# Kernel tuning notes

Hardware: AMD Instinct MI355X
Metric: run time of the kernel (lower is better)

The kernel has to match this reference:

```python
import jax, jax.numpy as jnp
import numpy as np

B, N = 8, 261888
PRE_NMS_LIMIT = 6000
PROPOSAL_COUNT = 1000
SCORE_THRES = 0.5
NMS_IOU_THRES = 0.7
RPN_BBOX_STD_DEV = jnp.asarray([0.1, 0.1, 0.2, 0.2], dtype=jnp.float32)
EPS = 1e-8


def setup_inputs() -> dict:
    key = jax.random.key(0)
    k1, k2, k3, k4 = jax.random.split(key, 4)
    # class scores: softmax over (negative, positive) logits
    logits = jax.random.normal(k1, (B, N, 2), dtype=jnp.float32)
    rpn_probs = jax.nn.softmax(logits, axis=-1)
    # raw (normalized) bbox deltas; layer multiplies by RPN_BBOX_STD_DEV
    rpn_bbox = jax.random.normal(k2, (B, N, 4), dtype=jnp.float32)
    # valid normalized anchors: y1<y2, x1<x2, roughly inside [0,1]
    ctr = jax.random.uniform(k3, (B, N, 2), minval=0.05, maxval=0.95, dtype=jnp.float32)
    size = jax.random.uniform(k4, (B, N, 2), minval=0.02, maxval=0.25, dtype=jnp.float32)
    anchors = jnp.concatenate([ctr - 0.5 * size, ctr + 0.5 * size], axis=-1)  # (y1,x1,y2,x2)
    return {"rpn_probs": rpn_probs, "rpn_bbox": rpn_bbox, "anchors": anchors}


def _apply_box_deltas(boxes, deltas):
    # boxes: [..., (y1,x1,y2,x2)], deltas: [..., (dy,dx,log(dh),log(dw))]
    h = boxes[..., 2] - boxes[..., 0]
    w = boxes[..., 3] - boxes[..., 1]
    cy = boxes[..., 0] + 0.5 * h
    cx = boxes[..., 1] + 0.5 * w
    cy = cy + deltas[..., 0] * h
    cx = cx + deltas[..., 1] * w
    h = h * jnp.exp(deltas[..., 2])
    w = w * jnp.exp(deltas[..., 3])
    y1 = cy - 0.5 * h
    x1 = cx - 0.5 * w
    return jnp.stack([y1, x1, y1 + h, x1 + w], axis=-1)


def _iou_one_vs_all(box, boxes, areas):
    # box: [4], boxes: [M,4], areas: [M]
    yy1 = jnp.maximum(box[0], boxes[:, 0])
    xx1 = jnp.maximum(box[1], boxes[:, 1])
    yy2 = jnp.minimum(box[2], boxes[:, 2])
    xx2 = jnp.minimum(box[3], boxes[:, 3])
    inter = jnp.maximum(yy2 - yy1, 0.0) * jnp.maximum(xx2 - xx1, 0.0)
    area_b = (box[2] - box[0]) * (box[3] - box[1])
    return inter / (area_b + areas - inter + EPS)


def _nms_single(boxes, scores):
    # boxes: [M,4] clipped to [0,1]; scores: [M]
    areas = (boxes[:, 2] - boxes[:, 0]) * (boxes[:, 3] - boxes[:, 1])
    live = jnp.where(scores >= SCORE_THRES, scores, -1.0)

    def step(s, _):
        idx = jnp.argmax(s)
        ok = s[idx] > 0.0
        box = boxes[idx]
        iou = _iou_one_vs_all(box, boxes, areas)
        s_new = jnp.where(iou >= NMS_IOU_THRES, -1.0, s)  # self has iou=1 -> suppressed
        s_new = s_new.at[idx].set(-1.0)
        out_box = jnp.where(ok, box, jnp.zeros((4,), boxes.dtype))
        return s_new, out_box

    _, picked = jax.lax.scan(step, live, None, length=PROPOSAL_COUNT)
    return picked  # [PROPOSAL_COUNT, 4], zero-padded


def reference(rpn_probs, rpn_bbox, anchors):
    scores = rpn_probs[..., 1]                                   # [B,N]
    deltas = rpn_bbox * RPN_BBOX_STD_DEV.reshape(1, 1, 4)        # [B,N,4]
    pre_nms = min(PRE_NMS_LIMIT, scores.shape[1])
    top_scores, ix = jax.lax.top_k(scores, pre_nms)              # [B,P]
    ix4 = ix[..., None]
    deltas_top = jnp.take_along_axis(deltas, ix4, axis=1)        # [B,P,4]
    anchors_top = jnp.take_along_axis(anchors, ix4, axis=1)      # [B,P,4]
    boxes = _apply_box_deltas(anchors_top, deltas_top)
    boxes = jnp.clip(boxes, 0.0, 1.0)                            # window (0,0,1,1)
    proposals = jax.vmap(_nms_single)(boxes, top_scores)         # [B,PROPOSAL_COUNT,4]
    return proposals
```

## Files before the change

kernel.cpp:

```cpp
#include <hip/hip_runtime.h>
#include <cstdint>
#include <cstddef>

#pragma clang fp contract(off)

#define BATCH    8
#define NANCH    261888
#define PRE_NMS  6000
#define PROP     1000
#define SORTN    8192
#define NSLOT    6144
#define MROW     96
#define NW       94
#define CHUNK_W  32
#define NZCAP    128
#define NPAIR    130944
#define CBLK     64
#define CPAIR    2046
#define KCAP     1024
#define SCORE_THRES_BITS 0x3F000000u
#define EPS_F    1e-8f
#define M_D      0.6999999582767486572265625

typedef unsigned long long ull;
typedef unsigned int u32;

__global__ __launch_bounds__(256)
void hist_kernel(const float* __restrict__ rpn_probs, u32* __restrict__ ghist,
                 u32* __restrict__ done, u32* __restrict__ Tc,
                 u32* __restrict__ binbase, u32* __restrict__ cntp)
{
    __shared__ u32 h[129];
    __shared__ u32 s_old;
    const int t = threadIdx.x;
    const int b = blockIdx.y;
    if (t < 129) h[t] = 0u;
    __syncthreads();

    const float4* p4 = reinterpret_cast<const float4*>(rpn_probs + (size_t)b * NANCH * 2);
    const int p0 = blockIdx.x * CPAIR;
    for (int i = t; i < CPAIR; i += 256) {
        float4 v = p4[p0 + i];
        u32 k0 = __float_as_uint(v.y);
        u32 k1 = __float_as_uint(v.w);
        if (k0 >= 0x3F000000u) atomicAdd(&h[min((k0 >> 16) - 0x3F00u, 128u)], 1u);
        if (k1 >= 0x3F000000u) atomicAdd(&h[min((k1 >> 16) - 0x3F00u, 128u)], 1u);
    }
    __syncthreads();
    if (t < 129 && h[t]) atomicAdd(&ghist[(b << 8) + t], h[t]);

    asm volatile("s_waitcnt vmcnt(0)" ::: "memory");
    if (t == 0) s_old = atomicAdd(&done[b], 1u);
    __syncthreads();
    if (s_old == CBLK - 1) {
        if (t < 129) h[t] = atomicAdd(&ghist[(b << 8) + t], 0u);
        __syncthreads();
        if (t == 0) {
            u32* bb = binbase + b * 132;
            u32 run = 0; int binT = -1; u32 Cv = 0;
            for (int i = 128; i >= 0; --i) {
                bb[i] = run;
                run += h[i];
                if (binT < 0 && run >= PRE_NMS) { binT = i; Cv = run; }
            }
            u32 T;
            if (binT < 0)         { T = 0x3F000000u; Cv = run; }
            else if (binT == 128)   T = 0x3F800000u;
            else                    T = 0x3F000000u + ((u32)binT << 16);
            Tc[b] = T;
            cntp[b << 6] = Cv;
        }
    }
}

__global__ __launch_bounds__(256)
void compact_kernel(const float* __restrict__ rpn_probs,
                    const u32* __restrict__ Tc,
                    const u32* __restrict__ binbase,
                    u32* __restrict__ bincnt,
                    ull* __restrict__ selbuf)
{
    __shared__ ull kbuf[KCAP];
    __shared__ u32 s_n;
    __shared__ u32 s_hist[132];
    __shared__ u32 s_base[132];
    const int t    = threadIdx.x;
    const int lane = t & 63;
    const int b    = blockIdx.y;
    const u32 T = Tc[b];
    const u32* bb = binbase + b * 132;
    u32* bc = bincnt + b * 132;
    if (t == 0) s_n = 0u;
    if (t < 132) s_hist[t] = 0u;
    __syncthreads();

    const float4* p4 = reinterpret_cast<const float4*>(rpn_probs + (size_t)b * NANCH * 2);
    ull* sb = selbuf + (size_t)b * SORTN;
    const int p0 = blockIdx.x * CPAIR;

    for (int i = t; i < CPAIR; i += 256) {
        float4 v = p4[p0 + i];
        const int n0 = (p0 + i) << 1;
        #pragma unroll
        for (int e = 0; e < 2; ++e) {
            u32 k = __float_as_uint(e ? v.w : v.y);
            bool s0 = (k >= T);
            ull m = __ballot(s0 ? 1 : 0);
            if (!m) continue;
            int ldr = __ffsll(m) - 1;
            u32 base = 0;
            if (lane == ldr) base = atomicAdd(&s_n, (u32)__popcll(m));
            base = __shfl(base, ldr);
            u32 off = base + (u32)__popcll(m & ((1ull << lane) - 1ull));
            if (s0) {
                ull pk = ((ull)(~k) << 32) | (ull)(u32)(n0 + e);
                if (off < KCAP) {
                    kbuf[off] = pk;
                } else {
                    u32 bin = min((k >> 16) - 0x3F00u, 128u);
                    u32 pos = bb[bin] + atomicAdd(&bc[bin], 1u);
                    if (pos < SORTN) sb[pos] = pk;
                }
            }
        }
    }
    __syncthreads();
    const u32 nn = min(s_n, (u32)KCAP);

    for (u32 j = t; j < nn; j += 256) {
        u32 k = ~(u32)(kbuf[j] >> 32);
        atomicAdd(&s_hist[min((k >> 16) - 0x3F00u, 128u)], 1u);
    }
    __syncthreads();

    if (t < 132 && s_hist[t]) s_base[t] = atomicAdd(&bc[t], s_hist[t]);
    __syncthreads();
    if (t < 132) s_hist[t] = 0u;
    __syncthreads();

    for (u32 j = t; j < nn; j += 256) {
        ull kv = kbuf[j];
        u32 k = ~(u32)(kv >> 32);
        u32 bin = min((k >> 16) - 0x3F00u, 128u);
        u32 local = atomicAdd(&s_hist[bin], 1u);
        u32 pos = bb[bin] + s_base[bin] + local;
        if (pos < SORTN) sb[pos] = kv;
    }
}

__global__ __launch_bounds__(256)
void rank_decode_kernel(const float* __restrict__ rpn_bbox,
                        const float* __restrict__ anchors,
                        const ull* __restrict__ selbuf,
                        const u32* __restrict__ cntp,
                        const u32* __restrict__ binbase,
                        const u32* __restrict__ ghist,
                        float4* __restrict__ boxes_ws,
                        float* __restrict__ area_ws,
                        ull* __restrict__ alive_ws)
{
    const int t = threadIdx.x;
    const int b = blockIdx.y;
    const u32 C = min(cntp[b << 6], (u32)SORTN);
    const ull* sb = selbuf + (size_t)b * SORTN;

    const int i = (blockIdx.x << 8) + t;
    if (i >= (int)C) return;

    const ull mykey = sb[i];
    const u32 key = ~(u32)(mykey >> 32);
    const u32 n   = (u32)(mykey & 0xFFFFFFFFull);
    const u32 bin = min((key >> 16) - 0x3F00u, 128u);
    const u32 lo  = binbase[b * 132 + bin];
    const u32 cb  = min(ghist[(b << 8) + bin], (u32)SORTN - lo);

    const ull* base = sb + lo;
    int local = 0;
    u32 j = 0;
    for (; j + 8 <= cb; j += 8) {
        #pragma unroll
        for (int u = 0; u < 8; ++u) local += (base[j + u] < mykey) ? 1 : 0;
    }
    for (; j < cb; ++j) local += (base[j] < mykey) ? 1 : 0;
    const int rank = (int)lo + local;

    if (rank < PRE_NMS) {
        const float4* bbox4 = reinterpret_cast<const float4*>(rpn_bbox + (size_t)b * NANCH * 4);
        const float4* anc4  = reinterpret_cast<const float4*>(anchors  + (size_t)b * NANCH * 4);
        float4 a = anc4[n];
        float4 d = bbox4[n];
        float dy = d.x * 0.1f, dx = d.y * 0.1f, dh = d.z * 0.2f, dw = d.w * 0.2f;
        float h  = a.z - a.x;
        float w  = a.w - a.y;
        float cy = a.x + 0.5f * h;
        float cx = a.y + 0.5f * w;
        cy = cy + dy * h;
        cx = cx + dx * w;
        h  = h * expf(dh);
        w  = w * expf(dw);
        float y1 = cy - 0.5f * h;
        float x1 = cx - 0.5f * w;
        float y2 = y1 + h;
        float x2 = x1 + w;
        y1 = fminf(fmaxf(y1, 0.f), 1.f);
        x1 = fminf(fmaxf(x1, 0.f), 1.f);
        y2 = fminf(fmaxf(y2, 0.f), 1.f);
        x2 = fminf(fmaxf(x2, 0.f), 1.f);
        boxes_ws[(size_t)b * NSLOT + rank] = make_float4(y1, x1, y2, x2);
        area_ws[(size_t)b * NSLOT + rank]  = (y2 - y1) * (x2 - x1);
        if (key >= SCORE_THRES_BITS) {
            atomicOr(&alive_ws[(size_t)b * MROW + (rank >> 6)], 1ull << (rank & 63));
        }
    }
}

__global__ __launch_bounds__(1024)
void iou_chunk_kernel(const float4* __restrict__ boxes_ws,
                      const float* __restrict__ area_ws,
                      ull* __restrict__ mat,
                      ull* __restrict__ nzmask,
                      const u32* __restrict__ flags,
                      int kend)
{
    const int b = blockIdx.y;
    if (flags && flags[b]) return;

    __shared__ float4 sbox[NSLOT];
    __shared__ float  sarea[NSLOT];

    const int j    = blockIdx.x;
    const int t    = threadIdx.x;
    const int lane = t & 63;
    const int wv   = t >> 6;

    const int kbeg = flags ? max(j, CHUNK_W) : j;
    const int base = j << 6;
    const int nst  = (kend << 6) - base;

    const float4* bws = boxes_ws + (size_t)b * NSLOT + base;
    const float*  aws = area_ws  + (size_t)b * NSLOT + base;
    for (int i = t; i < nst; i += 1024) { sbox[i] = bws[i]; sarea[i] = aws[i]; }
    __syncthreads();

    const int r0 = base + (wv << 2);
    if (r0 >= PRE_NMS) return;

    float4 P[4];
    float  PA[4];
    #pragma unroll
    for (int qi = 0; qi < 4; ++qi) { P[qi] = sbox[(wv << 2) + qi]; PA[qi] = sarea[(wv << 2) + qi]; }

    ull* rowp = mat + ((size_t)b * PRE_NMS + r0) * MROW;
    ull acc[4] = {0ull, 0ull, 0ull, 0ull};

    for (int k = kbeg; k < kend; ++k) {
        const int ci = ((k - j) << 6) + lane;
        const float4 qb = sbox[ci];
        const float  qa = sarea[ci];
        ull m[4];
        #pragma unroll
        for (int qi = 0; qi < 4; ++qi) {
            float yy1 = fmaxf(P[qi].x, qb.x);
            float xx1 = fmaxf(P[qi].y, qb.y);
            float yy2 = fminf(P[qi].z, qb.z);
            float xx2 = fminf(P[qi].w, qb.w);
            float inter = fmaxf(yy2 - yy1, 0.f) * fmaxf(xx2 - xx1, 0.f);
            float denom = ((PA[qi] + qa) - inter) + EPS_F;
            m[qi] = __ballot(((double)inter > M_D * (double)denom) ? 1 : 0);
        }
        if (k == j) {
            #pragma unroll
            for (int qi = 0; qi < 4; ++qi) {
                int sh = (wv << 2) + qi;
                ull keep = (sh == 63) ? 0ull : ((~0ull) << (sh + 1));
                m[qi] &= keep;
            }
        }
        #pragma unroll
        for (int qi = 0; qi < 4; ++qi) acc[qi] |= m[qi];
        if (lane == 0) {
            #pragma unroll
            for (int qi = 0; qi < 4; ++qi) rowp[(size_t)qi * MROW + k] = m[qi];
        }
    }

    if (lane == 0) {
        u32 bits = 0;
        #pragma unroll
        for (int qi = 0; qi < 4; ++qi) if (acc[qi]) bits |= 1u << qi;
        if (bits) atomicOr(&nzmask[(size_t)b * NW + j], (ull)bits << (wv << 2));
    }
}

__device__ __forceinline__ ull shfl_xor64(ull x, int s)
{
    return (ull)__shfl_xor((long long)x, s, 64);
}

__device__ __forceinline__ ull readlane64(ull x, int l)
{
    u32 lo = (u32)__builtin_amdgcn_readlane((int)(u32)x, l);
    u32 hi = (u32)__builtin_amdgcn_readlane((int)(u32)(x >> 32), l);
    return ((ull)hi << 32) | (ull)lo;
}

template<bool FIRST>
__global__ __launch_bounds__(64)
__attribute__((amdgpu_waves_per_eu(1, 1)))
void nms_scan_t(const float4* __restrict__ boxes_ws,
                const ull* __restrict__ alive_ws,
                const ull* __restrict__ mat,
                const ull* __restrict__ nzmask,
                float* __restrict__ out,
                u32* __restrict__ flags)
{
    const int b = blockIdx.x;
    if (!FIRST && flags[b]) return;

    const int lane = threadIdx.x;
    const int CW = FIRST ? CHUNK_W : NW;

    __shared__ int picks[PROP];
    __shared__ u32 nzrows[NZCAP];
    __shared__ __align__(16) ull nzbuf[NZCAP * 32];

    ull aw0 = 0, aw1 = 0;
    if (lane < 48) {
        const ull* aw = alive_ws + (size_t)b * MROW + 2 * lane;
        aw0 = aw[0]; aw1 = aw[1];
    }

    const ull* mb  = mat    + (size_t)b * PRE_NMS * MROW;
    const ull* nzm = nzmask + (size_t)b * NW;

    ull nzA = 0, nzB = 0;
    if (FIRST) { if (lane < CHUNK_W) nzA = nzm[lane]; }
    else       { if (lane < 47)      { nzA = nzm[2 * lane]; nzB = nzm[2 * lane + 1]; } }

    int excl = 0, NZ = 0;
    if (FIRST) {
        int c = (int)__popcll(nzA);
        int incl = c;
        for (int s = 1; s < 32; s <<= 1) {
            int y = __shfl_up(incl, s, 64);
            if (lane >= s) incl += y;
        }
        excl = incl - c;
        NZ = __builtin_amdgcn_readlane(incl, 31);

        {
            ull m = nzA; int r = excl;
            while (m) {
                int p = __ffsll(m) - 1; m &= m - 1ull;
                if (r < NZCAP) nzrows[r] = (u32)((lane << 6) + p);
                ++r;
            }
        }
        __syncthreads();

        const int NP = min(NZ, NZCAP);
        if (NP > 0) {
            u32 ridA = nzrows[lane];
            u32 ridB = nzrows[64 + lane];
            const int ninst = (NP + 3) >> 2;
            for (int i = 0; i < ninst; ++i) {
                int slot = 4 * i + (lane >> 4);
                if (slot >= NP) slot = NP - 1;
                int sel = (slot & 63) << 2;
                int ra = __builtin_amdgcn_ds_bpermute(sel, (int)ridA);
                int rb = __builtin_amdgcn_ds_bpermute(sel, (int)ridB);
                u32 rid = (u32)((slot < 64) ? ra : rb);
                const char* src = (const char*)(mb + (size_t)rid * MROW) + ((unsigned)(lane & 15) << 4);
                __builtin_amdgcn_global_load_lds(
                    (const __attribute__((address_space(1))) void*)src,
                    (__attribute__((address_space(3))) void*)((char*)&nzbuf[0] + i * 1024),
                    16, 0, 0);
            }
        }
        asm volatile("s_waitcnt vmcnt(0)" ::: "memory");
        __builtin_amdgcn_sched_barrier(0);
    }

    int cnt = 0;
    for (int k = 0; k < CW; ++k) {
        ull nzk;
        if (FIRST) nzk = readlane64(nzA, k);
        else       nzk = readlane64((k & 1) ? nzB : nzA, k >> 1);

        const int srcw = k >> 1;
        const ull awk = (k & 1) ? aw1 : aw0;
        ull wval = readlane64(awk, srcw);

        if (wval != 0ull) {
            const int slotbase_k = FIRST ? __builtin_amdgcn_readlane(excl, k) : 0;

            ull diag_cur = 0ull;
            if (nzk != 0ull) {
                bool mynz = (nzk >> lane) & 1ull;
                if (mynz) {
                    if (FIRST) {
                        int slot = slotbase_k + (int)__popcll(nzk & ((1ull << lane) - 1ull));
                        diag_cur = (slot < NZCAP) ? nzbuf[(size_t)slot * 32 + k]
                                                  : mb[(size_t)((k << 6) + lane) * MROW + k];
                    } else {
                        diag_cur = mb[(size_t)((k << 6) + lane) * MROW + k];
                    }
                }
            }

            const bool rowAlive = (wval >> lane) & 1ull;
            ull P;
            ull conflict = (nzk == 0ull) ? 0ull
                         : __ballot((rowAlive && ((diag_cur & wval) != 0ull)) ? 1 : 0);
            if (conflict == 0ull) {
                P = wval;
            } else {
                ull T = diag_cur;
                {
                    ull y;
                    y = shfl_xor64(T, 32);
                    T = (lane & 32) ? ((T & 0xFFFFFFFF00000000ull) | ((y & 0xFFFFFFFF00000000ull) >> 32))
                                    : ((T & 0x00000000FFFFFFFFull) | ((y & 0x00000000FFFFFFFFull) << 32));
                    y = shfl_xor64(T, 16);
                    T = (lane & 16) ? ((T & 0xFFFF0000FFFF0000ull) | ((y & 0xFFFF0000FFFF0000ull) >> 16))
                                    : ((T & 0x0000FFFF0000FFFFull) | ((y & 0x0000FFFF0000FFFFull) << 16));
                    y = shfl_xor64(T, 8);
                    T = (lane & 8)  ? ((T & 0xFF00FF00FF00FF00ull) | ((y & 0xFF00FF00FF00FF00ull) >> 8))
                                    : ((T & 0x00FF00FF00FF00FFull) | ((y & 0x00FF00FF00FF00FFull) << 8));
                    y = shfl_xor64(T, 4);
                    T = (lane & 4)  ? ((T & 0xF0F0F0F0F0F0F0F0ull) | ((y & 0xF0F0F0F0F0F0F0F0ull) >> 4))
                                    : ((T & 0x0F0F0F0F0F0F0F0Full) | ((y & 0x0F0F0F0F0F0F0F0Full) << 4));
                    y = shfl_xor64(T, 2);
                    T = (lane & 2)  ? ((T & 0xCCCCCCCCCCCCCCCCull) | ((y & 0xCCCCCCCCCCCCCCCCull) >> 2))
                                    : ((T & 0x3333333333333333ull) | ((y & 0x3333333333333333ull) << 2));
                    y = shfl_xor64(T, 1);
                    T = (lane & 1)  ? ((T & 0xAAAAAAAAAAAAAAAAull) | ((y & 0xAAAAAAAAAAAAAAAAull) >> 1))
                                    : ((T & 0x5555555555555555ull) | ((y & 0x5555555555555555ull) << 1));
                }
                ull A = wval;
                P = 0ull;
                while (A) {
                    const bool inA = (A >> lane) & 1ull;
                    ull D = __ballot((inA && ((T & A) == 0ull)) ? 1 : 0);
                    P |= D;
                    ull kill = __ballot((inA && ((T & D) != 0ull)) ? 1 : 0);
                    A &= ~(D | kill);
                }
            }

            const int total = __popcll(P);
            const int room  = PROP - cnt;
            const bool lanePicked = (P >> lane) & 1ull;
            const int myrank = __popcll(P & ((1ull << lane) - 1ull));
            if (lanePicked && myrank < room) picks[cnt + myrank] = (k << 6) + lane;
            cnt = (total >= room) ? PROP : (cnt + total);

            if (cnt < PROP && nzk != 0ull) {
                ull orset = P & nzk;
                while (orset) {
                    int p = __ffsll(orset) - 1; orset &= orset - 1ull;
                    ulonglong2 v;
                    if (FIRST) {
                        int slot = slotbase_k + (int)__popcll(nzk & ((1ull << p) - 1ull));
                        if (slot < NZCAP) {
                            const ulonglong2* bv = reinterpret_cast<const ulonglong2*>(&nzbuf[(size_t)slot * 32]);
                            v = bv[lane & 15];
                        } else {
                            const ulonglong2* gv = reinterpret_cast<const ulonglong2*>(mb + (size_t)((k << 6) + p) * MROW);
                            v = gv[lane & 15];
                        }
                    } else {
                        const ulonglong2* gv = reinterpret_cast<const ulonglong2*>(mb + (size_t)((k << 6) + p) * MROW);
                        v = gv[min(lane, 47)];
                    }
                    aw0 &= ~v.x; aw1 &= ~v.y;
                }
            }
        }

        if (lane == (k >> 1)) { if (k & 1) aw1 = 0ull; else aw0 = 0ull; }
        if (cnt == PROP) break;
    }

    __syncthreads();

    if (FIRST) {
        if (cnt != PROP) return;
        if (lane == 0) flags[b] = 1u;
    }

    const float4* bws = boxes_ws + (size_t)b * NSLOT;
    float4* ob = reinterpret_cast<float4*>(out + (size_t)b * PROP * 4);
    for (int i = lane; i < PROP; i += 64) {
        float4 v = make_float4(0.f, 0.f, 0.f, 0.f);
        if (i < cnt) v = bws[picks[i]];
        ob[i] = v;
    }
}

__device__ __forceinline__ void hist_add_f(unsigned int* hist, unsigned int bin, bool valid) {
    const int lane = threadIdx.x & 63;
    ull todo = __ballot(valid ? 1 : 0);
    #pragma unroll
    for (int it = 0; it < 3; ++it) {
        if (!todo) return;
        int leader = __ffsll(todo) - 1;
        unsigned int lbin = __shfl(bin, leader);
        ull grp = __ballot((valid && (bin == lbin)) ? 1 : 0);
        if (lane == leader) atomicAdd(&hist[lbin], (unsigned int)__popcll(grp));
        todo &= ~grp;
    }
    if ((todo >> lane) & 1ull) atomicAdd(&hist[bin], 1u);
}

__global__ __launch_bounds__(1024)
void proposal_fallback(const float* __restrict__ rpn_probs,
                       const float* __restrict__ rpn_bbox,
                       const float* __restrict__ anchors,
                       float* __restrict__ out)
{
    const int b    = blockIdx.x;
    const int t    = threadIdx.x;
    const int lane = t & 63;
    const int wv   = t >> 6;

    const float2* __restrict__ probs2 = reinterpret_cast<const float2*>(rpn_probs + (size_t)b * NANCH * 2);
    const float4* __restrict__ bbox4  = reinterpret_cast<const float4*>(rpn_bbox  + (size_t)b * NANCH * 4);
    const float4* __restrict__ anc4   = reinterpret_cast<const float4*>(anchors   + (size_t)b * NANCH * 4);
    float* __restrict__ outb = out + (size_t)b * PROP * 4;

    __shared__ __align__(16) char s_big[NSLOT * 16];
    __shared__ ull          s_alive[96];
    __shared__ unsigned int s_hist[256];
    __shared__ unsigned int s_pref;
    __shared__ unsigned int s_targ;
    __shared__ unsigned int s_cnt;

    ull*    sel   = reinterpret_cast<ull*>(s_big);
    float4* boxes = reinterpret_cast<float4*>(s_big);

    const int ITER = (NANCH + 1023) >> 10;

    if (t == 0) { s_pref = 0u; s_targ = PRE_NMS; s_cnt = 0u; }

    for (int p = 0; p < 4; ++p) {
        if (t < 256) s_hist[t] = 0u;
        __syncthreads();
        const unsigned int pref  = s_pref;
        const int          shift = 8 * (3 - p);
        const unsigned int pmask = (p == 0) ? 0u : (0xFFFFFFFFu << (shift + 8));
        for (int i = 0; i < ITER; ++i) {
            int  n     = (i << 10) + t;
            bool valid = (n < NANCH);
            unsigned int key = 0u;
            if (valid) key = __float_as_uint(probs2[n].y);
            bool match = valid && ((key & pmask) == (pref & pmask));
            hist_add_f(s_hist, (key >> shift) & 0xFFu, match);
        }
        __syncthreads();
        if (t == 0) {
            unsigned int target = s_targ;
            unsigned int acc = 0u;
            int v = 255;
            for (; v >= 0; --v) {
                unsigned int h = s_hist[v];
                if (acc + h >= target) break;
                acc += h;
            }
            if (v < 0) v = 0;
            s_pref = pref | ((unsigned int)v << shift);
            s_targ = target - acc;
        }
        __syncthreads();
    }

    const unsigned int T = s_pref;
    __syncthreads();

    for (int i = 0; i < ITER; ++i) {
        int  n     = (i << 10) + t;
        bool valid = (n < NANCH);
        unsigned int key = 0u;
        if (valid) key = __float_as_uint(probs2[n].y);
        bool selp = valid && (key >= T);
        ull  m    = __ballot(selp ? 1 : 0);
        if (m) {
            int leader = __ffsll(m) - 1;
            unsigned int base = 0u;
            if (lane == leader) base = atomicAdd(&s_cnt, (unsigned int)__popcll(m));
            base = __shfl(base, leader);
            if (selp) {
                unsigned int off = base + (unsigned int)__popcll(m & ((1ull << lane) - 1ull));
                if (off < SORTN) sel[off] = ((ull)(~key) << 32) | (ull)(unsigned int)n;
            }
        }
    }
    __syncthreads();
    const unsigned int C = s_cnt;
    for (int s = (int)C + t; s < SORTN; s += 1024) sel[s] = ~0ull;
    __syncthreads();

    for (unsigned int k = 2; k <= SORTN; k <<= 1) {
        for (unsigned int j = k >> 1; j > 0; j >>= 1) {
            #pragma unroll
            for (int r = 0; r < SORTN / 1024; ++r) {
                int i = (r << 10) + t;
                int l = i ^ (int)j;
                if (l > i) {
                    ull a  = sel[i];
                    ull bq = sel[l];
                    bool up = ((i & (int)k) == 0);
                    if ((a > bq) == up) { sel[i] = bq; sel[l] = a; }
                }
            }
            __syncthreads();
        }
    }

    ull ss[6];
    #pragma unroll
    for (int e = 0; e < 6; ++e) ss[e] = sel[(e << 10) + t];
    __syncthreads();

    float4 rbox[6];
    float  rarea[6];
    #pragma unroll
    for (int e = 0; e < 6; ++e) {
        int s = (e << 10) + t;
        float4 bx = make_float4(0.f, 0.f, 0.f, 0.f);
        bool ok = false;
        if (s < PRE_NMS) {
            unsigned int key = ~(unsigned int)(ss[e] >> 32);
            unsigned int n   = (unsigned int)(ss[e] & 0xFFFFFFFFull);
            float4 a = anc4[n];
            float4 d = bbox4[n];
            float dy = d.x * 0.1f, dx = d.y * 0.1f, dh = d.z * 0.2f, dw = d.w * 0.2f;
            float h  = a.z - a.x;
            float w  = a.w - a.y;
            float cy = a.x + 0.5f * h;
            float cx = a.y + 0.5f * w;
            cy = cy + dy * h;
            cx = cx + dx * w;
            h  = h * expf(dh);
            w  = w * expf(dw);
            float y1 = cy - 0.5f * h;
            float x1 = cx - 0.5f * w;
            float y2 = y1 + h;
            float x2 = x1 + w;
            y1 = fminf(fmaxf(y1, 0.f), 1.f);
            x1 = fminf(fmaxf(x1, 0.f), 1.f);
            y2 = fminf(fmaxf(y2, 0.f), 1.f);
            x2 = fminf(fmaxf(x2, 0.f), 1.f);
            bx = make_float4(y1, x1, y2, x2);
            ok = (key >= SCORE_THRES_BITS);
        }
        rbox[e]  = bx;
        rarea[e] = (bx.z - bx.x) * (bx.w - bx.y);
        boxes[s] = bx;
        ull am = __ballot(ok ? 1 : 0);
        if (lane == 0) s_alive[wv + (e << 4)] = am;
    }

    int emitted = 0;
    for (;;) {
        __syncthreads();
        if (emitted == PROP) break;
        ull w0 = s_alive[lane];
        ull w1 = (lane < 32) ? s_alive[64 + lane] : 0ull;
        ull nz0 = __ballot(w0 != 0ull ? 1 : 0);
        ull nz1 = __ballot(w1 != 0ull ? 1 : 0);
        int pick = -1;
        if (nz0) {
            int wd = __ffsll(nz0) - 1;
            ull wvv = __shfl(w0, wd);
            pick = (wd << 6) + __ffsll(wvv) - 1;
        } else if (nz1) {
            int wd = __ffsll(nz1) - 1;
            ull wvv = __shfl(w1, wd);
            pick = ((wd + 64) << 6) + __ffsll(wvv) - 1;
        }
        if (pick < 0) break;
        __syncthreads();

        if (t < 4) outb[(emitted << 2) + t] = reinterpret_cast<const float*>(s_big)[(pick << 2) + t];

        float4 p = boxes[pick];
        float parea = (p.z - p.x) * (p.w - p.y);
        #pragma unroll
        for (int e = 0; e < 6; ++e) {
            float4 bb  = rbox[e];
            float yy1 = fmaxf(p.x, bb.x);
            float xx1 = fmaxf(p.y, bb.y);
            float yy2 = fminf(p.z, bb.z);
            float xx2 = fminf(p.w, bb.w);
            float ih  = fmaxf(yy2 - yy1, 0.f);
            float iw  = fmaxf(xx2 - xx1, 0.f);
            float inter = ih * iw;
            float denom = ((parea + rarea[e]) - inter) + EPS_F;
            bool  sup   = ((double)inter > M_D * (double)denom);
            ull m = __ballot(sup ? 1 : 0);
            int word = wv + (e << 4);
            if (word == (pick >> 6)) m |= (1ull << (pick & 63));
            if (lane == 0) s_alive[word] &= ~m;
        }
        ++emitted;
    }

    for (int i = (emitted << 2) + t; i < PROP * 4; i += 1024) outb[i] = 0.f;
}

extern "C" void kernel_launch(void* const* d_in, const int* in_sizes, int n_in,
                              void* d_out, int out_size, void* d_ws, size_t ws_size,
                              hipStream_t stream) {
    const float* rpn_probs = (const float*)d_in[0];
    const float* rpn_bbox  = (const float*)d_in[1];
    const float* anchors   = (const float*)d_in[2];
    float* out = (float*)d_out;

    const size_t BOX_OFF   = 0;
    const size_t AREA_OFF  = 786432;
    const size_t ZERO_OFF  = 983040;
    const size_t ALIVE_OFF = 983040;
    const size_t TC_OFF    = 989184;
    const size_t DONE_OFF  = 989440;
    const size_t CNT_OFF   = 989696;
    const size_t GHIST_OFF = 991744;
    const size_t FLAG_OFF  = 999936;
    const size_t BINB_OFF  = 1000448;
    const size_t BINC_OFF  = 1004672;
    const size_t NZ_OFF    = 1008896;
    const size_t MAT_OFF   = 1u << 20;
    const size_t SELB_OFF  = MAT_OFF;
    const size_t WS_NEED   = MAT_OFF + (size_t)BATCH * PRE_NMS * MROW * 8;

    if (d_ws != nullptr && ws_size >= WS_NEED) {
        char* ws = (char*)d_ws;
        float4* boxes_ws = (float4*)(ws + BOX_OFF);
        float*  area_ws  = (float*)(ws + AREA_OFF);
        ull*    alive_ws = (ull*)(ws + ALIVE_OFF);
        u32*    Tc       = (u32*)(ws + TC_OFF);
        u32*    done     = (u32*)(ws + DONE_OFF);
        u32*    cntp     = (u32*)(ws + CNT_OFF);
        u32*    ghist    = (u32*)(ws + GHIST_OFF);
        u32*    flags    = (u32*)(ws + FLAG_OFF);
        u32*    binbase  = (u32*)(ws + BINB_OFF);
        u32*    bincnt   = (u32*)(ws + BINC_OFF);
        ull*    nzmask   = (ull*)(ws + NZ_OFF);
        ull*    selbuf   = (ull*)(ws + SELB_OFF);
        ull*    mat      = (ull*)(ws + MAT_OFF);

        hipMemsetAsync(ws + ZERO_OFF, 0, MAT_OFF - ZERO_OFF, stream);
        hipLaunchKernelGGL(hist_kernel, dim3(CBLK, BATCH), dim3(256), 0, stream,
                           rpn_probs, ghist, done, Tc, binbase, cntp);
        hipLaunchKernelGGL(compact_kernel, dim3(CBLK, BATCH), dim3(256), 0, stream,
                           rpn_probs, Tc, binbase, bincnt, selbuf);
        hipLaunchKernelGGL(rank_decode_kernel, dim3(SORTN / 256, BATCH), dim3(256), 0, stream,
                           rpn_bbox, anchors, selbuf, cntp, binbase, ghist,
                           boxes_ws, area_ws, alive_ws);
        hipLaunchKernelGGL(iou_chunk_kernel, dim3(CHUNK_W, BATCH), dim3(1024), 0, stream,
                           boxes_ws, area_ws, mat, nzmask, (const u32*)nullptr, CHUNK_W);
        hipLaunchKernelGGL((nms_scan_t<true>), dim3(BATCH), dim3(64), 0, stream,
                           boxes_ws, alive_ws, mat, nzmask, out, flags);
        hipLaunchKernelGGL(iou_chunk_kernel, dim3(NW, BATCH), dim3(1024), 0, stream,
                           boxes_ws, area_ws, mat, nzmask, (const u32*)flags, NW);
        hipLaunchKernelGGL((nms_scan_t<false>), dim3(BATCH), dim3(64), 0, stream,
                           boxes_ws, alive_ws, mat, nzmask, out, flags);
    } else {
        hipLaunchKernelGGL(proposal_fallback, dim3(BATCH), dim3(1024), 0, stream,
                           rpn_probs, rpn_bbox, anchors, out);
    }
}
```

Before: 202.4 us.

## Fuse fallback IoU pass and second NMS scan into one kernel with ticket barrier

Merges the second IoU-chunk kernel and the non-first NMS scan into a single rest_kernel. Each block computes its IoU rows, bumps a per-batch ticket, and block 0 spins until every block has arrived, then runs the scan. This removes one kernel launch and its inter-kernel gap. It relies on all NW blocks being co-resident, otherwise block 0 can wait forever, and block 0 carries the serial scan tail. The histogram and compact kernels also move from 256 to 512 threads per block.

```diff
diff --git a/kernel.cpp b/kernel.cpp
--- a/kernel.cpp
+++ b/kernel.cpp
@@ -25,21 +25,31 @@
 typedef unsigned long long ull;
 typedef unsigned int u32;
 
-__global__ __launch_bounds__(256)
+
+__device__ __forceinline__ void fence_release_agent()
+{
+    __builtin_amdgcn_fence(__ATOMIC_RELEASE, "agent");
+}
+__device__ __forceinline__ void fence_acquire_agent()
+{
+    __builtin_amdgcn_fence(__ATOMIC_ACQUIRE, "agent");
+}
+
+__global__ __launch_bounds__(512)
 void hist_kernel(const float* __restrict__ rpn_probs, u32* __restrict__ ghist,
                  u32* __restrict__ done, u32* __restrict__ Tc,
                  u32* __restrict__ binbase, u32* __restrict__ cntp)
 {
-    __shared__ u32 h[129];
+    __shared__ u32 h[132];
     __shared__ u32 s_old;
     const int t = threadIdx.x;
     const int b = blockIdx.y;
-    if (t < 129) h[t] = 0u;
+    if (t < 132) h[t] = 0u;
     __syncthreads();
 
     const float4* p4 = reinterpret_cast<const float4*>(rpn_probs + (size_t)b * NANCH * 2);
     const int p0 = blockIdx.x * CPAIR;
-    for (int i = t; i < CPAIR; i += 256) {
+    for (int i = t; i < CPAIR; i += 512) {
         float4 v = p4[p0 + i];
         u32 k0 = __float_as_uint(v.y);
         u32 k1 = __float_as_uint(v.w);
@@ -73,7 +83,7 @@
     }
 }
 
-__global__ __launch_bounds__(256)
+__global__ __launch_bounds__(512)
 void compact_kernel(const float* __restrict__ rpn_probs,
                     const u32* __restrict__ Tc,
                     const u32* __restrict__ binbase,
@@ -98,7 +108,7 @@
     ull* sb = selbuf + (size_t)b * SORTN;
     const int p0 = blockIdx.x * CPAIR;
 
-    for (int i = t; i < CPAIR; i += 256) {
+    for (int i = t; i < CPAIR; i += 512) {
         float4 v = p4[p0 + i];
         const int n0 = (p0 + i) << 1;
         #pragma unroll
@@ -127,7 +137,7 @@
     __syncthreads();
     const u32 nn = min(s_n, (u32)KCAP);
 
-    for (u32 j = t; j < nn; j += 256) {
+    for (u32 j = t; j < nn; j += 512) {
         u32 k = ~(u32)(kbuf[j] >> 32);
         atomicAdd(&s_hist[min((k >> 16) - 0x3F00u, 128u)], 1u);
     }
@@ -138,7 +148,7 @@
     if (t < 132) s_hist[t] = 0u;
     __syncthreads();
 
-    for (u32 j = t; j < nn; j += 256) {
+    for (u32 j = t; j < nn; j += 512) {
         ull kv = kbuf[j];
         u32 k = ~(u32)(kv >> 32);
         u32 bin = min((k >> 16) - 0x3F00u, 128u);
@@ -214,82 +224,84 @@
     }
 }
 
+__device__ void iou_block(const float4* __restrict__ bws_b,
+                          const float* __restrict__ aws_b,
+                          ull* __restrict__ mat_b, ull* __restrict__ nzm_b,
+                          int j, int kbeg, int kend,
+                          float4* sbox, float* sarea)
+{
+    const int t    = threadIdx.x;
+    const int lane = t & 63;
+    const int wv   = t >> 6;
+    const int base = j << 6;
+    const int nst  = (kend << 6) - base;
+
+    for (int i = t; i < nst; i += 1024) { sbox[i] = bws_b[base + i]; sarea[i] = aws_b[base + i]; }
+    __syncthreads();
+
+    const int r0 = base + (wv << 2);
+    if (r0 < PRE_NMS) {
+        float4 P[4];
+        float  PA[4];
+        #pragma unroll
+        for (int qi = 0; qi < 4; ++qi) { P[qi] = sbox[(wv << 2) + qi]; PA[qi] = sarea[(wv << 2) + qi]; }
+
+        ull* rowp = mat_b + (size_t)r0 * MROW;
+        ull acc[4] = {0ull, 0ull, 0ull, 0ull};
+
+        for (int k = kbeg; k < kend; ++k) {
+            const int ci = ((k - j) << 6) + lane;
+            const float4 qb = sbox[ci];
+            const float  qa = sarea[ci];
+            ull m[4];
+            #pragma unroll
+            for (int qi = 0; qi < 4; ++qi) {
+                float yy1 = fmaxf(P[qi].x, qb.x);
+                float xx1 = fmaxf(P[qi].y, qb.y);
+                float yy2 = fminf(P[qi].z, qb.z);
+                float xx2 = fminf(P[qi].w, qb.w);
+                float inter = fmaxf(yy2 - yy1, 0.f) * fmaxf(xx2 - xx1, 0.f);
+                float denom = ((PA[qi] + qa) - inter) + EPS_F;
+                m[qi] = __ballot(((double)inter > M_D * (double)denom) ? 1 : 0);
+            }
+            if (k == j) {
+                #pragma unroll
+                for (int qi = 0; qi < 4; ++qi) {
+                    int sh = (wv << 2) + qi;
+                    ull keep = (sh == 63) ? 0ull : ((~0ull) << (sh + 1));
+                    m[qi] &= keep;
+                }
+            }
+            #pragma unroll
+            for (int qi = 0; qi < 4; ++qi) acc[qi] |= m[qi];
+            if (lane == 0) {
+                #pragma unroll
+                for (int qi = 0; qi < 4; ++qi) rowp[(size_t)qi * MROW + k] = m[qi];
+            }
+        }
+
+        if (lane == 0) {
+            u32 bits = 0;
+            #pragma unroll
+            for (int qi = 0; qi < 4; ++qi) if (acc[qi]) bits |= 1u << qi;
+            if (bits) atomicOr(&nzm_b[j], (ull)bits << (wv << 2));
+        }
+    }
+    __syncthreads();
+}
+
 __global__ __launch_bounds__(1024)
 void iou_chunk_kernel(const float4* __restrict__ boxes_ws,
                       const float* __restrict__ area_ws,
                       ull* __restrict__ mat,
-                      ull* __restrict__ nzmask,
-                      const u32* __restrict__ flags,
-                      int kend)
+                      ull* __restrict__ nzmask)
 {
     const int b = blockIdx.y;
-    if (flags && flags[b]) return;
-
     __shared__ float4 sbox[NSLOT];
     __shared__ float  sarea[NSLOT];
-
-    const int j    = blockIdx.x;
-    const int t    = threadIdx.x;
-    const int lane = t & 63;
-    const int wv   = t >> 6;
-
-    const int kbeg = flags ? max(j, CHUNK_W) : j;
-    const int base = j << 6;
-    const int nst  = (kend << 6) - base;
-
-    const float4* bws = boxes_ws + (size_t)b * NSLOT + base;
-    const float*  aws = area_ws  + (size_t)b * NSLOT + base;
-    for (int i = t; i < nst; i += 1024) { sbox[i] = bws[i]; sarea[i] = aws[i]; }
-    __syncthreads();
-
-    const int r0 = base + (wv << 2);
-    if (r0 >= PRE_NMS) return;
-
-    float4 P[4];
-    float  PA[4];
-    #pragma unroll
-    for (int qi = 0; qi < 4; ++qi) { P[qi] = sbox[(wv << 2) + qi]; PA[qi] = sarea[(wv << 2) + qi]; }
-
-    ull* rowp = mat + ((size_t)b * PRE_NMS + r0) * MROW;
-    ull acc[4] = {0ull, 0ull, 0ull, 0ull};
-
-    for (int k = kbeg; k < kend; ++k) {
-        const int ci = ((k - j) << 6) + lane;
-        const float4 qb = sbox[ci];
-        const float  qa = sarea[ci];
-        ull m[4];
-        #pragma unroll
-        for (int qi = 0; qi < 4; ++qi) {
-            float yy1 = fmaxf(P[qi].x, qb.x);
-            float xx1 = fmaxf(P[qi].y, qb.y);
-            float yy2 = fminf(P[qi].z, qb.z);
-            float xx2 = fminf(P[qi].w, qb.w);
-            float inter = fmaxf(yy2 - yy1, 0.f) * fmaxf(xx2 - xx1, 0.f);
-            float denom = ((PA[qi] + qa) - inter) + EPS_F;
-            m[qi] = __ballot(((double)inter > M_D * (double)denom) ? 1 : 0);
-        }
-        if (k == j) {
-            #pragma unroll
-            for (int qi = 0; qi < 4; ++qi) {
-                int sh = (wv << 2) + qi;
-                ull keep = (sh == 63) ? 0ull : ((~0ull) << (sh + 1));
-                m[qi] &= keep;
-            }
-        }
-        #pragma unroll
-        for (int qi = 0; qi < 4; ++qi) acc[qi] |= m[qi];
-        if (lane == 0) {
-            #pragma unroll
-            for (int qi = 0; qi < 4; ++qi) rowp[(size_t)qi * MROW + k] = m[qi];
-        }
-    }
-
-    if (lane == 0) {
-        u32 bits = 0;
-        #pragma unroll
-        for (int qi = 0; qi < 4; ++qi) if (acc[qi]) bits |= 1u << qi;
-        if (bits) atomicOr(&nzmask[(size_t)b * NW + j], (ull)bits << (wv << 2));
-    }
+    iou_block(boxes_ws + (size_t)b * NSLOT, area_ws + (size_t)b * NSLOT,
+              mat + (size_t)b * PRE_NMS * MROW, nzmask + (size_t)b * NW,
+              blockIdx.x, blockIdx.x, CHUNK_W, sbox, sarea);
 }
 
 __device__ __forceinline__ ull shfl_xor64(ull x, int s)
@@ -305,33 +317,22 @@
 }
 
 template<bool FIRST>
-__global__ __launch_bounds__(64)
-__attribute__((amdgpu_waves_per_eu(1, 1)))
-void nms_scan_t(const float4* __restrict__ boxes_ws,
-                const ull* __restrict__ alive_ws,
-                const ull* __restrict__ mat,
-                const ull* __restrict__ nzmask,
-                float* __restrict__ out,
-                u32* __restrict__ flags)
-{
-    const int b = blockIdx.x;
-    if (!FIRST && flags[b]) return;
-
-    const int lane = threadIdx.x;
+__device__ void scan_wave(int b, int lane,
+                          const float4* __restrict__ bws_b,
+                          const ull* __restrict__ alive_ws,
+                          const ull* __restrict__ mb,
+                          const ull* __restrict__ nzm,
+                          float* __restrict__ out,
+                          u32* __restrict__ flags,
+                          int* picks, u32* nzrows, ull* nzbuf)
+{
     const int CW = FIRST ? CHUNK_W : NW;
-
-    __shared__ int picks[PROP];
-    __shared__ u32 nzrows[NZCAP];
-    __shared__ __align__(16) ull nzbuf[NZCAP * 32];
 
     ull aw0 = 0, aw1 = 0;
     if (lane < 48) {
         const ull* aw = alive_ws + (size_t)b * MROW + 2 * lane;
         aw0 = aw[0]; aw1 = aw[1];
     }
-
-    const ull* mb  = mat    + (size_t)b * PRE_NMS * MROW;
-    const ull* nzm = nzmask + (size_t)b * NW;
 
     ull nzA = 0, nzB = 0;
     if (FIRST) { if (lane < CHUNK_W) nzA = nzm[lane]; }
@@ -356,8 +357,6 @@
                 ++r;
             }
         }
-        __syncthreads();
-
         const int NP = min(NZ, NZCAP);
         if (NP > 0) {
             u32 ridA = nzrows[lane];
@@ -373,7 +372,7 @@
                 const char* src = (const char*)(mb + (size_t)rid * MROW) + ((unsigned)(lane & 15) << 4);
                 __builtin_amdgcn_global_load_lds(
                     (const __attribute__((address_space(1))) void*)src,
-                    (__attribute__((address_space(3))) void*)((char*)&nzbuf[0] + i * 1024),
+                    (__attribute__((address_space(3))) void*)((char*)nzbuf + i * 1024),
                     16, 0, 0);
             }
         }
@@ -415,35 +414,35 @@
             if (conflict == 0ull) {
                 P = wval;
             } else {
-                ull T = diag_cur;
+                ull Tt = diag_cur;
                 {
                     ull y;
-                    y = shfl_xor64(T, 32);
-                    T = (lane & 32) ? ((T & 0xFFFFFFFF00000000ull) | ((y & 0xFFFFFFFF00000000ull) >> 32))
-                                    : ((T & 0x00000000FFFFFFFFull) | ((y & 0x00000000FFFFFFFFull) << 32));
-                    y = shfl_xor64(T, 16);
-                    T = (lane & 16) ? ((T & 0xFFFF0000FFFF0000ull) | ((y & 0xFFFF0000FFFF0000ull) >> 16))
-                                    : ((T & 0x0000FFFF0000FFFFull) | ((y & 0x0000FFFF0000FFFFull) << 16));
-                    y = shfl_xor64(T, 8);
-                    T = (lane & 8)  ? ((T & 0xFF00FF00FF00FF00ull) | ((y & 0xFF00FF00FF00FF00ull) >> 8))
-                                    : ((T & 0x00FF00FF00FF00FFull) | ((y & 0x00FF00FF00FF00FFull) << 8));
-                    y = shfl_xor64(T, 4);
-                    T = (lane & 4)  ? ((T & 0xF0F0F0F0F0F0F0F0ull) | ((y & 0xF0F0F0F0F0F0F0F0ull) >> 4))
-                                    : ((T & 0x0F0F0F0F0F0F0F0Full) | ((y & 0x0F0F0F0F0F0F0F0Full) << 4));
-                    y = shfl_xor64(T, 2);
-                    T = (lane & 2)  ? ((T & 0xCCCCCCCCCCCCCCCCull) | ((y & 0xCCCCCCCCCCCCCCCCull) >> 2))
-                                    : ((T & 0x3333333333333333ull) | ((y & 0x3333333333333333ull) << 2));
-                    y = shfl_xor64(T, 1);
-                    T = (lane & 1)  ? ((T & 0xAAAAAAAAAAAAAAAAull) | ((y & 0xAAAAAAAAAAAAAAAAull) >> 1))
-                                    : ((T & 0x5555555555555555ull) | ((y & 0x5555555555555555ull) << 1));
+                    y = shfl_xor64(Tt, 32);
+                    Tt = (lane & 32) ? ((Tt & 0xFFFFFFFF00000000ull) | ((y & 0xFFFFFFFF00000000ull) >> 32))
+                                     : ((Tt & 0x00000000FFFFFFFFull) | ((y & 0x00000000FFFFFFFFull) << 32));
+                    y = shfl_xor64(Tt, 16);
+                    Tt = (lane & 16) ? ((Tt & 0xFFFF0000FFFF0000ull) | ((y & 0xFFFF0000FFFF0000ull) >> 16))
+                                     : ((Tt & 0x0000FFFF0000FFFFull) | ((y & 0x0000FFFF0000FFFFull) << 16));
+                    y = shfl_xor64(Tt, 8);
+                    Tt = (lane & 8)  ? ((Tt & 0xFF00FF00FF00FF00ull) | ((y & 0xFF00FF00FF00FF00ull) >> 8))
+                                     : ((Tt & 0x00FF00FF00FF00FFull) | ((y & 0x00FF00FF00FF00FFull) << 8));
+                    y = shfl_xor64(Tt, 4);
+                    Tt = (lane & 4)  ? ((Tt & 0xF0F0F0F0F0F0F0F0ull) | ((y & 0xF0F0F0F0F0F0F0F0ull) >> 4))
+                                     : ((Tt & 0x0F0F0F0F0F0F0F0Full) | ((y & 0x0F0F0F0F0F0F0F0Full) << 4));
+                    y = shfl_xor64(Tt, 2);
+                    Tt = (lane & 2)  ? ((Tt & 0xCCCCCCCCCCCCCCCCull) | ((y & 0xCCCCCCCCCCCCCCCCull) >> 2))
+                                     : ((Tt & 0x3333333333333333ull) | ((y & 0x3333333333333333ull) << 2));
+                    y = shfl_xor64(Tt, 1);
+                    Tt = (lane & 1)  ? ((Tt & 0xAAAAAAAAAAAAAAAAull) | ((y & 0xAAAAAAAAAAAAAAAAull) >> 1))
+                                     : ((Tt & 0x5555555555555555ull) | ((y & 0x5555555555555555ull) << 1));
                 }
                 ull A = wval;
                 P = 0ull;
                 while (A) {
                     const bool inA = (A >> lane) & 1ull;
-                    ull D = __ballot((inA && ((T & A) == 0ull)) ? 1 : 0);
+                    ull D = __ballot((inA && ((Tt & A) == 0ull)) ? 1 : 0);
                     P |= D;
-                    ull kill = __ballot((inA && ((T & D) != 0ull)) ? 1 : 0);
+                    ull kill = __ballot((inA && ((Tt & D) != 0ull)) ? 1 : 0);
                     A &= ~(D | kill);
                 }
             }
@@ -463,7 +462,7 @@
                     if (FIRST) {
                         int slot = slotbase_k + (int)__popcll(nzk & ((1ull << p) - 1ull));
                         if (slot < NZCAP) {
-                            const ulonglong2* bv = reinterpret_cast<const ulonglong2*>(&nzbuf[(size_t)slot * 32]);
+                            const ulonglong2* bv = reinterpret_cast<const ulonglong2*>(nzbuf + (size_t)slot * 32);
                             v = bv[lane & 15];
                         } else {
                             const ulonglong2* gv = reinterpret_cast<const ulonglong2*>(mb + (size_t)((k << 6) + p) * MROW);
@@ -482,19 +481,75 @@
         if (cnt == PROP) break;
     }
 
-    __syncthreads();
-
     if (FIRST) {
-        if (cnt != PROP) return;
-        if (lane == 0) flags[b] = 1u;
-    }
-
-    const float4* bws = boxes_ws + (size_t)b * NSLOT;
+        if (cnt != PROP) {
+            if (lane == 0) atomicExch(&flags[b], 2u);
+            return;
+        }
+        if (lane == 0) atomicExch(&flags[b], 1u);
+    }
+
     float4* ob = reinterpret_cast<float4*>(out + (size_t)b * PROP * 4);
     for (int i = lane; i < PROP; i += 64) {
         float4 v = make_float4(0.f, 0.f, 0.f, 0.f);
-        if (i < cnt) v = bws[picks[i]];
+        if (i < cnt) v = bws_b[picks[i]];
         ob[i] = v;
+    }
+}
+
+__global__ __launch_bounds__(64)
+__attribute__((amdgpu_waves_per_eu(1, 1)))
+void scanA_kernel(const float4* __restrict__ boxes_ws,
+                  const ull* __restrict__ alive_ws,
+                  const ull* __restrict__ mat,
+                  const ull* __restrict__ nzmask,
+                  float* __restrict__ out,
+                  u32* __restrict__ flags)
+{
+    const int b = blockIdx.x;
+    __shared__ int picks[PROP];
+    __shared__ u32 nzrows[NZCAP];
+    __shared__ __align__(16) ull nzbuf[NZCAP * 32];
+    scan_wave<true>(b, threadIdx.x, boxes_ws + (size_t)b * NSLOT, alive_ws,
+                    mat + (size_t)b * PRE_NMS * MROW, nzmask + (size_t)b * NW,
+                    out, flags, picks, nzrows, nzbuf);
+}
+
+__global__ __launch_bounds__(1024)
+void rest_kernel(const float4* __restrict__ boxes_ws,
+                 const float* __restrict__ area_ws,
+                 ull* __restrict__ mat, ull* __restrict__ nzmask,
+                 const ull* __restrict__ alive_ws,
+                 u32* __restrict__ flags, u32* __restrict__ ticket4,
+                 float* __restrict__ out)
+{
+    const int b  = blockIdx.y;
+    if (flags[b] == 1u) return;
+
+    const int jj = blockIdx.x;
+    const int t  = threadIdx.x;
+
+    __shared__ float4 sbox[NSLOT];
+    __shared__ float  sarea[NSLOT];
+    __shared__ int    picks[PROP];
+    __shared__ u32    nzrows[NZCAP];
+
+    const float4* bws_b = boxes_ws + (size_t)b * NSLOT;
+    const float*  aws_b = area_ws  + (size_t)b * NSLOT;
+    ull* mat_b = mat    + (size_t)b * PRE_NMS * MROW;
+    ull* nzm_b = nzmask + (size_t)b * NW;
+
+    iou_block(bws_b, aws_b, mat_b, nzm_b, jj, max(jj, (int)CHUNK_W), NW, sbox, sarea);
+    fence_release_agent();
+    if (t == 0) atomicAdd(&ticket4[b], 1u);
+
+    if (jj == 0 && t < 64) {
+        if (t == 0) {
+            while (atomicAdd(&ticket4[b], 0u) < (u32)NW) __builtin_amdgcn_s_sleep(8);
+        }
+        fence_acquire_agent();
+        scan_wave<false>(b, t, bws_b, alive_ws, mat_b, nzm_b, out, flags,
+                         picks, nzrows, (ull*)nullptr);
     }
 }
 
@@ -729,6 +784,7 @@
     const size_t BINB_OFF  = 1000448;
     const size_t BINC_OFF  = 1004672;
     const size_t NZ_OFF    = 1008896;
+    const size_t TK4_OFF   = 1015936;
     const size_t MAT_OFF   = 1u << 20;
     const size_t SELB_OFF  = MAT_OFF;
     const size_t WS_NEED   = MAT_OFF + (size_t)BATCH * PRE_NMS * MROW * 8;
@@ -746,25 +802,25 @@
         u32*    binbase  = (u32*)(ws + BINB_OFF);
         u32*    bincnt   = (u32*)(ws + BINC_OFF);
         ull*    nzmask   = (ull*)(ws + NZ_OFF);
+        u32*    ticket4  = (u32*)(ws + TK4_OFF);
         ull*    selbuf   = (ull*)(ws + SELB_OFF);
         ull*    mat      = (ull*)(ws + MAT_OFF);
 
         hipMemsetAsync(ws + ZERO_OFF, 0, MAT_OFF - ZERO_OFF, stream);
-        hipLaunchKernelGGL(hist_kernel, dim3(CBLK, BATCH), dim3(256), 0, stream,
+        hipLaunchKernelGGL(hist_kernel, dim3(CBLK, BATCH), dim3(512), 0, stream,
                            rpn_probs, ghist, done, Tc, binbase, cntp);
-        hipLaunchKernelGGL(compact_kernel, dim3(CBLK, BATCH), dim3(256), 0, stream,
+        hipLaunchKernelGGL(compact_kernel, dim3(CBLK, BATCH), dim3(512), 0, stream,
                            rpn_probs, Tc, binbase, bincnt, selbuf);
         hipLaunchKernelGGL(rank_decode_kernel, dim3(SORTN / 256, BATCH), dim3(256), 0, stream,
                            rpn_bbox, anchors, selbuf, cntp, binbase, ghist,
                            boxes_ws, area_ws, alive_ws);
         hipLaunchKernelGGL(iou_chunk_kernel, dim3(CHUNK_W, BATCH), dim3(1024), 0, stream,
-                           boxes_ws, area_ws, mat, nzmask, (const u32*)nullptr, CHUNK_W);
-        hipLaunchKernelGGL((nms_scan_t<true>), dim3(BATCH), dim3(64), 0, stream,
+                           boxes_ws, area_ws, mat, nzmask);
+        hipLaunchKernelGGL(scanA_kernel, dim3(BATCH), dim3(64), 0, stream,
                            boxes_ws, alive_ws, mat, nzmask, out, flags);
-        hipLaunchKernelGGL(iou_chunk_kernel, dim3(NW, BATCH), dim3(1024), 0, stream,
-                           boxes_ws, area_ws, mat, nzmask, (const u32*)flags, NW);
-        hipLaunchKernelGGL((nms_scan_t<false>), dim3(BATCH), dim3(64), 0, stream,
-                           boxes_ws, alive_ws, mat, nzmask, out, flags);
+        hipLaunchKernelGGL(rest_kernel, dim3(NW, BATCH), dim3(1024), 0, stream,
+                           boxes_ws, area_ws, mat, nzmask, alive_ws,
+                           flags, ticket4, out);
     } else {
         hipLaunchKernelGGL(proposal_fallback, dim3(BATCH), dim3(1024), 0, stream,
                            rpn_probs, rpn_bbox, anchors, out);
```

Result: faster. 198.4 us (-2.0%).
